# Kernel optimization log

Hardware: AMD Instinct MI355X
Metric: run time of the kernel (lower is better)

The kernel has to match this reference:

```python
import jax, jax.numpy as jnp
from jax import lax
import numpy as np
import math

MAXV = 127.0  # 2**(8-1)-1, signed int8 narrow range

def setup_inputs() -> dict:
    key = jax.random.key(0)
    kx, kw, kb = jax.random.split(key, 3)
    B, Cin, H, W = 32, 128, 56, 56
    Cout, K = 256, 3
    x = jax.random.normal(kx, (B, Cin, H, W), dtype=jnp.float32)
    # kaiming_uniform_(a=sqrt(5)) -> bound = sqrt(6 / ((1+5) * fan_in)) = 1/sqrt(fan_in)
    fan_in = Cin * K * K
    bound = 1.0 / math.sqrt(fan_in)
    weight = jax.random.uniform(kw, (Cout, Cin, K, K), dtype=jnp.float32,
                                minval=-bound, maxval=bound)
    bias = jax.random.uniform(kb, (Cout,), dtype=jnp.float32,
                              minval=-bound, maxval=bound)
    return {"x": x, "weight": weight, "bias": bias}

def _quantize_i8(t):
    """Max-calibrated signed 8-bit quantization (fake_quant=False -> integer output)."""
    amax = jnp.max(jnp.abs(t))
    scale = MAXV / amax
    q = jnp.clip(jnp.round(t * scale), -MAXV, MAXV).astype(jnp.int8)
    return q, scale

def reference(x, weight, bias):
    # quantize activations and weights to int8
    qx, sx = _quantize_i8(x)
    qw, sw = _quantize_i8(weight)
    # exact int8 conv with int32 accumulation (systolic exact path), stride=1, pad=1
    out_i32 = lax.conv_general_dilated(
        qx, qw,
        window_strides=(1, 1),
        padding=((1, 1), (1, 1)),
        dimension_numbers=("NCHW", "OIHW", "NCHW"),
        preferred_element_type=jnp.int32,
    )
    # dequantize and add bias
    out = out_i32.astype(jnp.float32) / (sx * sw)
    return out + bias[None, :, None, None]
```

## Files before the change

kernel.cpp:

```cpp
#include <hip/hip_runtime.h>
#include <hip/hip_bf16.h>


#define B_    32
#define CIN   128
#define H_    56
#define W_    56
#define COUT  256
#define HP    58
#define WP    58
#define HWP   (H_*W_)
#define NPIX  (B_*HWP)
#define NCHUNK 18
#define CHUNK_BYTES (COUT*64)

typedef int int4v __attribute__((ext_vector_type(4)));

__device__ __forceinline__ void gld_lds16(const void* g, void* l) {
    __builtin_amdgcn_global_load_lds(
        (const __attribute__((address_space(1))) unsigned int*)g,
        (__attribute__((address_space(3))) unsigned int*)l, 16, 0, 0);
}

__global__ __launch_bounds__(256) void pad_zero_kernel(signed char* __restrict__ xq,
                                                       unsigned* __restrict__ scales) {
    const int b = blockIdx.x;
    if (b == 0 && threadIdx.x < 2) scales[threadIdx.x] = 0;
    int4* base = (int4*)(xq + (long)b * HP * WP * CIN);
    const int ROWI4 = WP * CIN / 16;
    int4 z; z.x = 0; z.y = 0; z.z = 0; z.w = 0;
    for (int i = threadIdx.x; i < ROWI4; i += 256) base[i] = z;
    int4* top = base + 57 * ROWI4;
    for (int i = threadIdx.x; i < ROWI4; i += 256) top[i] = z;
    for (int idx = threadIdx.x; idx < 56 * 16; idx += 256) {
        const int h = idx >> 4, c = idx & 15;
        const int w = (c < 8) ? 0 : 57, p = c & 7;
        base[(h + 1) * ROWI4 + w * (CIN / 16) + p] = z;
    }
}

__global__ __launch_bounds__(256) void amax_kernel(const float4* __restrict__ x, long n4x,
                                                   const float4* __restrict__ wt, long n4w,
                                                   unsigned* __restrict__ scales) {
    const float4* p; long n4; unsigned* slot; long start, stride;
    if (blockIdx.x < 2048) {
        p = x; n4 = n4x; slot = scales;
        start = (long)blockIdx.x * 256 + threadIdx.x; stride = 2048L * 256;
    } else {
        p = wt; n4 = n4w; slot = scales + 1;
        start = (long)(blockIdx.x - 2048) * 256 + threadIdx.x; stride = 128L * 256;
    }
    float m = 0.f;
    for (long i = start; i < n4; i += stride) {
        float4 v = p[i];
        m = fmaxf(m, fmaxf(fmaxf(fabsf(v.x), fabsf(v.y)), fmaxf(fabsf(v.z), fabsf(v.w))));
    }
    __shared__ float red[256];
    red[threadIdx.x] = m; __syncthreads();
    for (int s = 128; s > 0; s >>= 1) {
        if (threadIdx.x < s) red[threadIdx.x] = fmaxf(red[threadIdx.x], red[threadIdx.x + s]);
        __syncthreads();
    }
    if (threadIdx.x == 0) atomicMax(slot, __float_as_uint(red[0]));
}

__global__ __launch_bounds__(256) void quant_x_kernel(const float* __restrict__ x,
        const unsigned* __restrict__ scales, signed char* __restrict__ xq) {
    const int bh = blockIdx.x;
    const int b = bh / H_, h = bh % H_;
    const float sx = 127.0f / __uint_as_float(scales[0]);
    __shared__ int ldsq[W_ * 33];
    const int tid = threadIdx.x;
    const int w = tid & 63;
    const int chi = tid >> 6;
    if (w < W_) {
        const float* xb = x + (long)b * CIN * HWP + h * W_ + w;
#pragma unroll
        for (int it = 0; it < 8; ++it) {
            const int c4 = it * 4 + chi;
            int pk = 0;
#pragma unroll
            for (int u = 0; u < 4; ++u) {
                float v = xb[(long)(c4 * 4 + u) * HWP];
                float q = fminf(127.f, fmaxf(-127.f, rintf(v * sx)));
                pk |= ((int)q & 0xff) << (u * 8);
            }
            ldsq[w * 33 + c4] = pk;
        }
    }
    __syncthreads();
    int4* dst = (int4*)(xq + (((long)b * HP + h + 1) * WP + 1) * CIN);
    for (int idx = tid; idx < W_ * 8; idx += 256) {
        const int ww = idx >> 3, c16 = idx & 7;
        int4 v;
        v.x = ldsq[ww * 33 + c16 * 4 + 0];
        v.y = ldsq[ww * 33 + c16 * 4 + 1];
        v.z = ldsq[ww * 33 + c16 * 4 + 2];
        v.w = ldsq[ww * 33 + c16 * 4 + 3];
        dst[ww * 8 + c16] = v;
    }
}

__global__ __launch_bounds__(256) void quant_w_kernel(const float* __restrict__ wt,
        const unsigned* __restrict__ scales, signed char* __restrict__ wq) {
    const int id = blockIdx.x * 256 + threadIdx.x;
    if (id >= COUT * 9 * 32) return;
    const float sw = 127.0f / __uint_as_float(scales[1]);
    const int co = id / 288;
    const int r  = id % 288;
    const int t  = r / 32;
    const int c4 = r % 32;
    int pk = 0;
#pragma unroll
    for (int u = 0; u < 4; ++u) {
        float v = wt[(co * CIN + c4 * 4 + u) * 9 + t];
        float q = fminf(127.f, fmaxf(-127.f, rintf(v * sw)));
        pk |= ((int)q & 0xff) << (u * 8);
    }
    const int k = t * CIN + c4 * 4;
    const int chunk = k >> 6;
    const int off = k & 63;
    *(int*)(wq + (long)chunk * CHUNK_BYTES + co * 64 + off) = pk;
}

__global__ __launch_bounds__(512, 4) void conv_kernel(
        const signed char* __restrict__ xq, const signed char* __restrict__ wq,
        const float* __restrict__ bias, const unsigned* __restrict__ scales,
        float* __restrict__ out) {
    __shared__ signed char As[2][16384];
    __shared__ signed char Bs[2][8192];

    const int tid = threadIdx.x;
    const int lane = tid & 63;
    const int wv = tid >> 6;
    const int ln = lane & 15;
    const int g  = lane >> 4;

    const int wco = wv >> 1;
    const int wpx = wv & 1;
    const int px_blk = blockIdx.x * 128;

    const int e0 = wv * 2, e1 = e0 + 1;
    const int gA0 = e0 >> 2, qA0 = e0 & 3;
    const int gA1 = e1 >> 2, qA1 = e1 & 3;
    const signed char* srcA0 = wq + (qA0 * 64 + lane) * 64 + gA0 * 16;
    const signed char* srcA1 = wq + (qA1 * 64 + lane) * 64 + gA1 * 16;
    const int ldsA0 = gA0 * 4096 + qA0 * 1024 + lane * 16;
    const int ldsA1 = gA1 * 4096 + qA1 * 1024 + lane * 16;

    const int gB = wv >> 1, halfB = wv & 1;
    const int pxs = px_blk + halfB * 64 + lane;
    const int bS = pxs / HWP, hwS = pxs % HWP;
    const int hS = hwS / W_, wS = hwS % W_;
    const signed char* srcB = xq + ((bS * HP + hS) * WP + wS) * CIN + gB * 16;
    const int ldsB = gB * 2048 + halfB * 1024 + lane * 16;

#define STAGE(c, buf) { \
    const int tap_ = (c) >> 1; \
    const int toff_ = ((tap_ / 3) * WP + (tap_ % 3)) * CIN + ((c) & 1) * 64; \
    gld_lds16(srcA0 + (c) * CHUNK_BYTES, &As[buf][ldsA0]); \
    gld_lds16(srcA1 + (c) * CHUNK_BYTES, &As[buf][ldsA1]); \
    gld_lds16(srcB + toff_, &Bs[buf][ldsB]); }

    int4v acc[4][4] = {};
    STAGE(0, 0);
#pragma unroll
    for (int c = 0; c < NCHUNK; ++c) {
        const int cur = c & 1;
        __syncthreads();
        if (c + 1 < NCHUNK) STAGE(c + 1, cur ^ 1);
        int4v Af[4], Bf[4];
#pragma unroll
        for (int i = 0; i < 4; ++i)
            Af[i] = *(const int4v*)&As[cur][g * 4096 + (wco * 64 + i * 16 + ln) * 16];
#pragma unroll
        for (int j = 0; j < 4; ++j)
            Bf[j] = *(const int4v*)&Bs[cur][g * 2048 + (wpx * 64 + j * 16 + ln) * 16];
#pragma unroll
        for (int i = 0; i < 4; ++i)
#pragma unroll
            for (int j = 0; j < 4; ++j)
                acc[i][j] = __builtin_amdgcn_mfma_i32_16x16x64_i8(Af[i], Bf[j], acc[i][j], 0, 0, 0);
    }
#undef STAGE

    const float ax = __uint_as_float(scales[0]);
    const float aw = __uint_as_float(scales[1]);
    const float inv = 1.0f / ((127.0f / ax) * (127.0f / aw));

#pragma unroll
    for (int i = 0; i < 4; ++i) {
        const int co = wco * 64 + i * 16 + g * 4;
#pragma unroll
        for (int r = 0; r < 4; ++r) {
            const float bsv = bias[co + r];
#pragma unroll
            for (int j = 0; j < 4; ++j) {
                const int px = px_blk + wpx * 64 + j * 16 + ln;
                const int b = px / HWP, hw = px % HWP;
                out[((long)(b * COUT + co + r)) * HWP + hw] = (float)acc[i][j][r] * inv + bsv;
            }
        }
    }
}

extern "C" void kernel_launch(void* const* d_in, const int* in_sizes, int n_in,
                              void* d_out, int out_size, void* d_ws, size_t ws_size,
                              hipStream_t stream) {
    const float* x  = (const float*)d_in[0];
    const float* wt = (const float*)d_in[1];
    const float* bs = (const float*)d_in[2];
    float* out = (float*)d_out;

    unsigned* scales = (unsigned*)d_ws;
    const size_t XQ_OFF   = 256;
    const size_t XQ_BYTES = (size_t)B_ * HP * WP * CIN;
    signed char* xq = (signed char*)d_ws + XQ_OFF;
    signed char* wq = xq + XQ_BYTES;

    pad_zero_kernel<<<B_, 256, 0, stream>>>(xq, scales);

    const long n4x = (long)B_ * CIN * H_ * W_ / 4;
    const long n4w = (long)COUT * CIN * 9 / 4;
    amax_kernel<<<2176, 256, 0, stream>>>((const float4*)x, n4x, (const float4*)wt, n4w, scales);

    quant_x_kernel<<<B_ * H_, 256, 0, stream>>>(x, scales, xq);
    quant_w_kernel<<<(COUT * 9 * 32 + 255) / 256, 256, 0, stream>>>(wt, scales, wq);

    conv_kernel<<<NPIX / 128, 512, 0, stream>>>(xq, wq, bs, scales, out);
}
```

Baseline: 219.2 us.

## Triple-buffer conv K-loop with split barriers, pre-swizzled weights, and fused padding

Moves the conv main loop from double to triple buffering so the load for chunk c+2 is issued while chunk c computes. It waits with explicit vmcnt and barriers and splits the MFMA work into two halves with a mid barrier and setprio. Weights are stored in the exact LDS layout so the A tile is a straight copy, and blocks are remapped across the grid. Padding zeroing moves into the quant_x kernel and the scale reset becomes a memset, removing one kernel launch. The cost is more LDS per block (72KB), which may reduce occupancy.

```diff
diff --git a/kernel.cpp b/kernel.cpp
--- a/kernel.cpp
+++ b/kernel.cpp
@@ -1,5 +1,4 @@
 #include <hip/hip_runtime.h>
-#include <hip/hip_bf16.h>
 
 
 #define B_    32
@@ -12,7 +11,7 @@
 #define HWP   (H_*W_)
 #define NPIX  (B_*HWP)
 #define NCHUNK 18
-#define CHUNK_BYTES (COUT*64)
+#define ACHUNK 16384
 
 typedef int int4v __attribute__((ext_vector_type(4)));
 
@@ -20,23 +19,6 @@
     __builtin_amdgcn_global_load_lds(
         (const __attribute__((address_space(1))) unsigned int*)g,
         (__attribute__((address_space(3))) unsigned int*)l, 16, 0, 0);
-}
-
-__global__ __launch_bounds__(256) void pad_zero_kernel(signed char* __restrict__ xq,
-                                                       unsigned* __restrict__ scales) {
-    const int b = blockIdx.x;
-    if (b == 0 && threadIdx.x < 2) scales[threadIdx.x] = 0;
-    int4* base = (int4*)(xq + (long)b * HP * WP * CIN);
-    const int ROWI4 = WP * CIN / 16;
-    int4 z; z.x = 0; z.y = 0; z.z = 0; z.w = 0;
-    for (int i = threadIdx.x; i < ROWI4; i += 256) base[i] = z;
-    int4* top = base + 57 * ROWI4;
-    for (int i = threadIdx.x; i < ROWI4; i += 256) top[i] = z;
-    for (int idx = threadIdx.x; idx < 56 * 16; idx += 256) {
-        const int h = idx >> 4, c = idx & 15;
-        const int w = (c < 8) ? 0 : 57, p = c & 7;
-        base[(h + 1) * ROWI4 + w * (CIN / 16) + p] = z;
-    }
 }
 
 __global__ __launch_bounds__(256) void amax_kernel(const float4* __restrict__ x, long n4x,
@@ -71,6 +53,19 @@
     const float sx = 127.0f / __uint_as_float(scales[0]);
     __shared__ int ldsq[W_ * 33];
     const int tid = threadIdx.x;
+
+    int4 z; z.x = 0; z.y = 0; z.z = 0; z.w = 0;
+    int4* prow = (int4*)(xq + ((long)b * HP + h + 1) * WP * CIN);
+    if (tid < 8) prow[tid] = z;
+    else if (tid < 16) prow[456 + tid - 8] = z;
+    if (h == 0) {
+        int4* r0 = (int4*)(xq + (long)b * HP * WP * CIN);
+        for (int i = tid; i < 464; i += 256) r0[i] = z;
+    } else if (h == H_ - 1) {
+        int4* rt = (int4*)(xq + ((long)b * HP + 57) * WP * CIN);
+        for (int i = tid; i < 464; i += 256) rt[i] = z;
+    }
+
     const int w = tid & 63;
     const int chi = tid >> 6;
     if (w < W_) {
@@ -120,15 +115,15 @@
     const int k = t * CIN + c4 * 4;
     const int chunk = k >> 6;
     const int off = k & 63;
-    *(int*)(wq + (long)chunk * CHUNK_BYTES + co * 64 + off) = pk;
+    *(int*)(wq + (long)chunk * ACHUNK + (off >> 4) * 4096 + co * 16 + (off & 15)) = pk;
 }
 
 __global__ __launch_bounds__(512, 4) void conv_kernel(
         const signed char* __restrict__ xq, const signed char* __restrict__ wq,
         const float* __restrict__ bias, const unsigned* __restrict__ scales,
         float* __restrict__ out) {
-    __shared__ signed char As[2][16384];
-    __shared__ signed char Bs[2][8192];
+    __shared__ signed char As[3][16384];
+    __shared__ signed char Bs[3][8192];
 
     const int tid = threadIdx.x;
     const int lane = tid & 63;
@@ -138,15 +133,13 @@
 
     const int wco = wv >> 1;
     const int wpx = wv & 1;
-    const int px_blk = blockIdx.x * 128;
-
-    const int e0 = wv * 2, e1 = e0 + 1;
-    const int gA0 = e0 >> 2, qA0 = e0 & 3;
-    const int gA1 = e1 >> 2, qA1 = e1 & 3;
-    const signed char* srcA0 = wq + (qA0 * 64 + lane) * 64 + gA0 * 16;
-    const signed char* srcA1 = wq + (qA1 * 64 + lane) * 64 + gA1 * 16;
-    const int ldsA0 = gA0 * 4096 + qA0 * 1024 + lane * 16;
-    const int ldsA1 = gA1 * 4096 + qA1 * 1024 + lane * 16;
+
+    const int bid = blockIdx.x;
+    const int wg  = (bid & 7) * 98 + (bid >> 3);
+    const int px_blk = wg * 128;
+
+    const int aoff0 = wv * 2048 + lane * 16;
+    const int aoff1 = aoff0 + 1024;
 
     const int gB = wv >> 1, halfB = wv & 1;
     const int pxs = px_blk + halfB * 64 + lane;
@@ -155,33 +148,47 @@
     const signed char* srcB = xq + ((bS * HP + hS) * WP + wS) * CIN + gB * 16;
     const int ldsB = gB * 2048 + halfB * 1024 + lane * 16;
 
-#define STAGE(c, buf) { \
+#define STAGE(c) { \
     const int tap_ = (c) >> 1; \
     const int toff_ = ((tap_ / 3) * WP + (tap_ % 3)) * CIN + ((c) & 1) * 64; \
-    gld_lds16(srcA0 + (c) * CHUNK_BYTES, &As[buf][ldsA0]); \
-    gld_lds16(srcA1 + (c) * CHUNK_BYTES, &As[buf][ldsA1]); \
-    gld_lds16(srcB + toff_, &Bs[buf][ldsB]); }
+    const int bf_ = (c) % 3; \
+    gld_lds16(wq + (c) * ACHUNK + aoff0, &As[bf_][aoff0]); \
+    gld_lds16(wq + (c) * ACHUNK + aoff1, &As[bf_][aoff1]); \
+    gld_lds16(srcB + toff_, &Bs[bf_][ldsB]); }
+
+#define LDA_(i) (*(const int4v*)&As[buf][g * 4096 + (wco * 64 + (i) * 16 + ln) * 16])
+#define LDB_(j) (*(const int4v*)&Bs[buf][g * 2048 + (wpx * 64 + (j) * 16 + ln) * 16])
+#define MM(i, j, A, Bv) acc[i][j] = __builtin_amdgcn_mfma_i32_16x16x64_i8(A, Bv, acc[i][j], 0, 0, 0)
+
+#define CHUNK(c, VM) { \
+    const int buf = (c) % 3; \
+    asm volatile("s_waitcnt vmcnt(" #VM ")\n\ts_barrier" ::: "memory"); \
+    __builtin_amdgcn_sched_barrier(0); \
+    if ((c) + 2 < NCHUNK) STAGE((c) + 2); \
+    int4v Bf0 = LDB_(0), Bf1 = LDB_(1), Bf2 = LDB_(2), Bf3 = LDB_(3); \
+    int4v Af0 = LDA_(0), Af1 = LDA_(1); \
+    __builtin_amdgcn_s_setprio(1); \
+    MM(0, 0, Af0, Bf0); MM(0, 1, Af0, Bf1); MM(0, 2, Af0, Bf2); MM(0, 3, Af0, Bf3); \
+    MM(1, 0, Af1, Bf0); MM(1, 1, Af1, Bf1); MM(1, 2, Af1, Bf2); MM(1, 3, Af1, Bf3); \
+    __builtin_amdgcn_s_setprio(0); \
+    asm volatile("s_barrier" ::: "memory"); \
+    __builtin_amdgcn_sched_barrier(0); \
+    int4v Af2 = LDA_(2), Af3 = LDA_(3); \
+    __builtin_amdgcn_s_setprio(1); \
+    MM(2, 0, Af2, Bf0); MM(2, 1, Af2, Bf1); MM(2, 2, Af2, Bf2); MM(2, 3, Af2, Bf3); \
+    MM(3, 0, Af3, Bf0); MM(3, 1, Af3, Bf1); MM(3, 2, Af3, Bf2); MM(3, 3, Af3, Bf3); \
+    __builtin_amdgcn_s_setprio(0); }
 
     int4v acc[4][4] = {};
-    STAGE(0, 0);
-#pragma unroll
-    for (int c = 0; c < NCHUNK; ++c) {
-        const int cur = c & 1;
-        __syncthreads();
-        if (c + 1 < NCHUNK) STAGE(c + 1, cur ^ 1);
-        int4v Af[4], Bf[4];
-#pragma unroll
-        for (int i = 0; i < 4; ++i)
-            Af[i] = *(const int4v*)&As[cur][g * 4096 + (wco * 64 + i * 16 + ln) * 16];
-#pragma unroll
-        for (int j = 0; j < 4; ++j)
-            Bf[j] = *(const int4v*)&Bs[cur][g * 2048 + (wpx * 64 + j * 16 + ln) * 16];
-#pragma unroll
-        for (int i = 0; i < 4; ++i)
-#pragma unroll
-            for (int j = 0; j < 4; ++j)
-                acc[i][j] = __builtin_amdgcn_mfma_i32_16x16x64_i8(Af[i], Bf[j], acc[i][j], 0, 0, 0);
-    }
+    STAGE(0);
+    STAGE(1);
+    CHUNK(0, 3)  CHUNK(1, 3)  CHUNK(2, 3)  CHUNK(3, 3)  CHUNK(4, 3)  CHUNK(5, 3)
+    CHUNK(6, 3)  CHUNK(7, 3)  CHUNK(8, 3)  CHUNK(9, 3)  CHUNK(10, 3) CHUNK(11, 3)
+    CHUNK(12, 3) CHUNK(13, 3) CHUNK(14, 3) CHUNK(15, 3) CHUNK(16, 3) CHUNK(17, 0)
+#undef CHUNK
+#undef MM
+#undef LDA_
+#undef LDB_
 #undef STAGE
 
     const float ax = __uint_as_float(scales[0]);
@@ -218,7 +225,7 @@
     signed char* xq = (signed char*)d_ws + XQ_OFF;
     signed char* wq = xq + XQ_BYTES;
 
-    pad_zero_kernel<<<B_, 256, 0, stream>>>(xq, scales);
+    hipMemsetAsync(d_ws, 0, 8, stream);
 
     const long n4x = (long)B_ * CIN * H_ * W_ / 4;
     const long n4w = (long)COUT * CIN * 9 / 4;
```

Measured after the change: 214.6 us. 2.1% less time.
